# Optimization experiments

Measured on AMD Instinct MI355X. Metric: run time of the kernel, lower is better.

Reference implementation:

```python
import jax
import jax.numpy as jnp
import numpy as np

# Module configuration (matches init_kwargs)
N, C, H, W = 8, 256, 64, 64
CO, KH, KW = 256, 3, 3
SH, SW = 1, 1
PH, PW = 1, 1
DH, DW = 1, 1
G, DG = 1, 1
K = KH * KW
HO = (H + 2 * PH - (DH * (KH - 1) + 1)) // SH + 1
WO = (W + 2 * PW - (DW * (KW - 1) + 1)) // SW + 1


def setup_inputs() -> dict:
    key = jax.random.key(0)
    k1, k2, k3, k4 = jax.random.split(key, 4)
    x = jax.random.normal(k1, (N, C, H, W), dtype=jnp.float32)
    offset = jax.random.normal(k2, (N, DG * 2 * K, HO, WO), dtype=jnp.float32)
    mask = jax.random.uniform(k3, (N, DG * K, HO, WO), dtype=jnp.float32)
    stdv = 1.0 / np.sqrt(C * KH * KW)
    weight = jax.random.uniform(k4, (CO, C // G, KH, KW), dtype=jnp.float32,
                                minval=-stdv, maxval=stdv)
    return {"x": x, "offset": offset, "mask": mask, "weight": weight}


def _deform_sample(x, offset, mask):
    """Modulated deformable bilinear sampling (DCNv2 im2col).

    Returns columns [N, C, K, HO, WO].
    """
    Cg = C // DG
    # offset layout: [N, DG, K, 2(y,x), HO, WO]
    off = offset.reshape(N, DG, K, 2, HO, WO)
    off_y, off_x = off[:, :, :, 0], off[:, :, :, 1]

    # Base sampling grid per kernel tap: [K, HO, WO] broadcastable
    kgy = (jnp.repeat(jnp.arange(KH), KW) * DH).astype(jnp.float32)  # [K]
    kgx = (jnp.tile(jnp.arange(KW), KH) * DW).astype(jnp.float32)    # [K]
    oy = (jnp.arange(HO) * SH - PH).astype(jnp.float32)              # [HO]
    ox = (jnp.arange(WO) * SW - PW).astype(jnp.float32)              # [WO]
    py = kgy[:, None, None] + oy[None, :, None] + off_y  # [N,DG,K,HO,WO]
    px = kgx[:, None, None] + ox[None, None, :] + off_x  # [N,DG,K,HO,WO]

    y0 = jnp.floor(py)
    x0 = jnp.floor(px)
    ly = py - y0
    lx = px - x0
    y0i = y0.astype(jnp.int32)
    x0i = x0.astype(jnp.int32)
    y1i = y0i + 1
    x1i = x0i + 1

    xf = x.reshape(N, DG, Cg, H * W)

    def gather_one(xf_nd, idx_nd):
        # xf_nd: [Cg, H*W], idx_nd: [K*HO*WO] -> [Cg, K*HO*WO]
        return xf_nd[:, idx_nd]

    gather = jax.vmap(jax.vmap(gather_one))  # over N, DG

    def corner(yi, xi, wgt):
        valid = (yi >= 0) & (yi < H) & (xi >= 0) & (xi < W)
        yc = jnp.clip(yi, 0, H - 1)
        xc = jnp.clip(xi, 0, W - 1)
        idx = (yc * W + xc).reshape(N, DG, K * HO * WO)
        g = gather(xf, idx).reshape(N, DG, Cg, K, HO, WO)
        w = (wgt * valid.astype(x.dtype))[:, :, None]  # [N,DG,1,K,HO,WO]
        return g * w

    cols = corner(y0i, x0i, (1.0 - ly) * (1.0 - lx))
    cols = cols + corner(y0i, x1i, (1.0 - ly) * lx)
    cols = cols + corner(y1i, x0i, ly * (1.0 - lx))
    cols = cols + corner(y1i, x1i, ly * lx)

    # modulation
    m = mask.reshape(N, DG, 1, K, HO, WO)
    cols = cols * m
    return cols.reshape(N, C, K, HO, WO)


def reference(x, offset, mask, weight):
    cols = _deform_sample(x, offset, mask)              # [N,C,K,HO,WO]
    colsg = cols.reshape(N, G, C // G, K, HO, WO)
    wg = weight.reshape(G, CO // G, C // G, K)
    out = jnp.einsum('ngckhw,gock->ngohw', colsg, wg)
    return out.reshape(N, CO, HO, WO)
```

## Files before the change

### kernel.cpp

```cpp
#include <hip/hip_runtime.h>
#include <hip/hip_bf16.h>
#include <hip/hip_fp16.h>
#include <stdint.h>

#define N_   8
#define C_   256
#define H_   64
#define W_   64
#define CO_  256
#define K_   9
#define HO_  64
#define WO_  64
#define CK_  (C_ * K_)
#define P_   (HO_ * WO_)

#define BN   128
#define BK   64
#define NT   36
#define NTHR 512

typedef __attribute__((ext_vector_type(8))) _Float16 f16x8;
typedef __attribute__((ext_vector_type(4))) float f32x4;

__device__ __forceinline__ unsigned short f2bf(float f) {
    uint32_t u = __builtin_bit_cast(uint32_t, f);
    uint32_t r = (u + 0x7FFFu + ((u >> 16) & 1u)) >> 16;
    return (unsigned short)r;
}
__device__ __forceinline__ float bf2f(unsigned short u) {
    return __builtin_bit_cast(float, (uint32_t)u << 16);
}
__device__ __forceinline__ unsigned short f2h(float f) {
    return __builtin_bit_cast(unsigned short, (_Float16)f);
}


__global__ __launch_bounds__(256)
void transpose_x(const float* __restrict__ x, unsigned short* __restrict__ xT) {
    __shared__ float t[64][65];
    const int n  = blockIdx.z;
    const int c0 = blockIdx.y * 64;
    const int h0 = blockIdx.x * 64;
    const int tx = threadIdx.x & 63;
    const int ty = threadIdx.x >> 6;
    const float* xp = x + ((size_t)n * C_ + c0) * P_ + h0;
    #pragma unroll
    for (int i = 0; i < 16; ++i) {
        int c = ty * 16 + i;
        t[c][tx] = xp[(size_t)c * P_ + tx];
    }
    __syncthreads();
    unsigned short* op = xT + ((size_t)n * P_ + h0) * C_ + c0;
    #pragma unroll
    for (int i = 0; i < 16; ++i) {
        int hw = ty * 16 + i;
        op[(size_t)hw * C_ + tx] = f2h(t[tx][hw]);
    }
}

__global__ __launch_bounds__(256)
void reorder_w(const float* __restrict__ w, unsigned short* __restrict__ Wt) {
    const int co = blockIdx.x;
    const int c  = threadIdx.x;
    const float* src = w + (size_t)co * CK_ + (size_t)c * K_;
    float v[9];
    #pragma unroll
    for (int k = 0; k < 9; ++k) v[k] = src[k];
    #pragma unroll
    for (int k = 0; k < 9; ++k)
        Wt[(size_t)co * CK_ + k * C_ + c] = f2h(v[k]);
}

__device__ __forceinline__ void barrier_lgkm_only() {
    __builtin_amdgcn_sched_barrier(0);
    asm volatile("s_waitcnt lgkmcnt(0)" ::: "memory");
    __builtin_amdgcn_s_barrier();
    __builtin_amdgcn_sched_barrier(0);
}

#define COMB(dst, A, B, Cc, D) do {                                   \
    __half2 _v = __hmul2(W0, __builtin_bit_cast(__half2, (A)));       \
    _v = __hfma2(W1, __builtin_bit_cast(__half2, (B)), _v);           \
    _v = __hfma2(W2, __builtin_bit_cast(__half2, (Cc)), _v);          \
    _v = __hfma2(W3, __builtin_bit_cast(__half2, (D)), _v);           \
    (dst) = __builtin_bit_cast(unsigned, _v); } while (0)

__global__ __launch_bounds__(NTHR, 2)
void dcn_main(const unsigned short* __restrict__ xT,
              const unsigned short* __restrict__ Wt,
              const float* __restrict__ offset,
              const float* __restrict__ mask,
              float* __restrict__ out) {
    __shared__ uint2 sIdx[BN * K_];
    __shared__ uint4 sWd [BN * K_];
    __shared__ unsigned short sWs[2][CO_ * BK];
    __shared__ unsigned short sBs[2][BN * BK];

    const int tid = threadIdx.x;
    const int bid = blockIdx.x;
    const int n   = bid & 7;
    const int p0  = (bid >> 3) * BN;

    for (int e = tid; e < BN * K_; e += NTHR) {
        int pl = e / K_;
        int k  = e - pl * K_;
        int p  = p0 + pl;
        int ho = p >> 6, wo = p & 63;
        float offy = offset[(size_t)((n * 2 * K_ + 2 * k)     * P_) + p];
        float offx = offset[(size_t)((n * 2 * K_ + 2 * k + 1) * P_) + p];
        float m    = mask  [(size_t)((n * K_ + k) * P_) + p];
        float py = (float)(k / 3 + ho - 1) + offy;
        float px = (float)(k % 3 + wo - 1) + offx;
        float y0f = floorf(py), x0f = floorf(px);
        float ly = py - y0f,   lx = px - x0f;
        int y0 = (int)y0f, x0 = (int)x0f;
        int y1 = y0 + 1,   x1 = x0 + 1;
        bool vy0 = (y0 >= 0) & (y0 < H_);
        bool vy1 = (y1 >= 0) & (y1 < H_);
        bool vx0 = (x0 >= 0) & (x0 < W_);
        bool vx1 = (x1 >= 0) & (x1 < W_);
        float w00 = (1.f - ly) * (1.f - lx) * m * ((vy0 & vx0) ? 1.f : 0.f);
        float w01 = (1.f - ly) * lx         * m * ((vy0 & vx1) ? 1.f : 0.f);
        float w10 = ly * (1.f - lx)         * m * ((vy1 & vx0) ? 1.f : 0.f);
        float w11 = ly * lx                 * m * ((vy1 & vx1) ? 1.f : 0.f);
        unsigned int cy0 = (unsigned)min(max(y0, 0), H_ - 1);
        unsigned int cy1 = (unsigned)min(max(y1, 0), H_ - 1);
        unsigned int cx0 = (unsigned)min(max(x0, 0), W_ - 1);
        unsigned int cx1 = (unsigned)min(max(x1, 0), W_ - 1);
        sIdx[e] = make_uint2((cy0 * W_ + cx0) | ((cy0 * W_ + cx1) << 16),
                             (cy1 * W_ + cx0) | ((cy1 * W_ + cx1) << 16));
        sWd[e] = make_uint4((unsigned)f2h(w00) * 0x10001u,
                            (unsigned)f2h(w01) * 0x10001u,
                            (unsigned)f2h(w10) * 0x10001u,
                            (unsigned)f2h(w11) * 0x10001u);
    }
    __syncthreads();

    const unsigned short* xTn = xT + (size_t)n * P_ * C_;

    const int spl  = tid >> 2;
    const int cs16 = (tid & 3) * 16;
    const int bsw  = spl & 7;
    const int boff0 = spl * 128 + ((((tid & 3) * 2)     ^ bsw) << 4);
    const int boff1 = spl * 128 + ((((tid & 3) * 2 + 1) ^ bsw) << 4);
    const int wco  = tid >> 1;
    const int wchq = (tid & 1) * 4;
    const int wswz = wco & 7;
    const int woff = wco * 128;
    const unsigned short* wsrcbase = Wt + (size_t)wco * CK_ + (tid & 1) * 32;

    const int lane = tid & 63;
    const int wid  = tid >> 6;
    const int wm   = (wid & 3) * 64;
    const int wp   = (wid >> 2) * 64;
    const int l15  = lane & 15;
    const int l4   = lane >> 4;
    const int slA  = l4 ^ (l15 & 7);

    f32x4 acc[4][4] = {};

    uint4 qa0, qa1, qb0, qb1, qc0, qc1, qd0, qd1;
    uint4 wq0, wq1, wq2, wq3;

#define PREF(TT) {                                                        \
        const int kn  = (TT) >> 2;                                        \
        const int c0n = ((TT) & 3) * 64;                                  \
        const unsigned short* ws = wsrcbase + kn * C_ + c0n;              \
        wq0 = *(const uint4*)(ws);                                        \
        wq1 = *(const uint4*)(ws + 8);                                    \
        wq2 = *(const uint4*)(ws + 16);                                   \
        wq3 = *(const uint4*)(ws + 24);                                   \
        uint2 id = sIdx[spl * K_ + kn];                                   \
        const unsigned short* base = xTn + c0n + cs16;                    \
        const unsigned short* ba = base + ((size_t)(id.x & 0xFFFFu) << 8);\
        const unsigned short* bb = base + ((size_t)(id.x >> 16)     << 8);\
        const unsigned short* bc = base + ((size_t)(id.y & 0xFFFFu) << 8);\
        const unsigned short* bd = base + ((size_t)(id.y >> 16)     << 8);\
        qa0 = *(const uint4*)(ba); qa1 = *(const uint4*)(ba + 8);         \
        qb0 = *(const uint4*)(bb); qb1 = *(const uint4*)(bb + 8);         \
        qc0 = *(const uint4*)(bc); qc1 = *(const uint4*)(bc + 8);         \
        qd0 = *(const uint4*)(bd); qd1 = *(const uint4*)(bd + 8);         \
    }

#define STAGE(TT, WB, BB) {                                               \
        asm volatile("s_waitcnt vmcnt(0)" ::: "memory");                  \
        char* wrB = (char*)(WB) + woff;                                   \
        *(uint4*)(wrB + (((wchq + 0) ^ wswz) << 4)) = wq0;                \
        *(uint4*)(wrB + (((wchq + 1) ^ wswz) << 4)) = wq1;                \
        *(uint4*)(wrB + (((wchq + 2) ^ wswz) << 4)) = wq2;                \
        *(uint4*)(wrB + (((wchq + 3) ^ wswz) << 4)) = wq3;                \
        uint4 wv = sWd[spl * K_ + ((TT) >> 2)];                           \
        __half2 W0 = __builtin_bit_cast(__half2, wv.x);                   \
        __half2 W1 = __builtin_bit_cast(__half2, wv.y);                   \
        __half2 W2 = __builtin_bit_cast(__half2, wv.z);                   \
        __half2 W3 = __builtin_bit_cast(__half2, wv.w);                   \
        uint4 r0, r1;                                                     \
        COMB(r0.x, qa0.x, qb0.x, qc0.x, qd0.x);                           \
        COMB(r0.y, qa0.y, qb0.y, qc0.y, qd0.y);                           \
        COMB(r0.z, qa0.z, qb0.z, qc0.z, qd0.z);                           \
        COMB(r0.w, qa0.w, qb0.w, qc0.w, qd0.w);                           \
        COMB(r1.x, qa1.x, qb1.x, qc1.x, qd1.x);                           \
        COMB(r1.y, qa1.y, qb1.y, qc1.y, qd1.y);                           \
        COMB(r1.z, qa1.z, qb1.z, qc1.z, qd1.z);                           \
        COMB(r1.w, qa1.w, qb1.w, qc1.w, qd1.w);                           \
        *(uint4*)((char*)(BB) + boff0) = r0;                              \
        *(uint4*)((char*)(BB) + boff1) = r1;                              \
    }

    PREF(0)
    STAGE(0, sWs[0], sBs[0])
    PREF(1)

    for (int t = 0; t < NT; ++t) {
        const int br = t & 1;
        const int bw = br ^ 1;
        const char* wR = (const char*)sWs[br];
        const char* bR = (const char*)sBs[br];

        barrier_lgkm_only();

        f16x8 a0[2], a1[2], a2[2], a3[2], b0[2], b1[2], b2[2], b3[2];
        {
            const int sl = slA;
            b0[0] = *(const f16x8*)(bR + (wp      + l15) * 128 + (sl << 4));
            b1[0] = *(const f16x8*)(bR + (wp + 16 + l15) * 128 + (sl << 4));
            b2[0] = *(const f16x8*)(bR + (wp + 32 + l15) * 128 + (sl << 4));
            b3[0] = *(const f16x8*)(bR + (wp + 48 + l15) * 128 + (sl << 4));
            a0[0] = *(const f16x8*)(wR + (wm      + l15) * 128 + (sl << 4));
            a1[0] = *(const f16x8*)(wR + (wm + 16 + l15) * 128 + (sl << 4));
            a2[0] = *(const f16x8*)(wR + (wm + 32 + l15) * 128 + (sl << 4));
            a3[0] = *(const f16x8*)(wR + (wm + 48 + l15) * 128 + (sl << 4));
        }

        if (t + 1 < NT) {
            if (br) { STAGE(t + 1, sWs[0], sBs[0]) }
            else    { STAGE(t + 1, sWs[1], sBs[1]) }
            if (t + 2 < NT) PREF(t + 2)
        }

        {
            const int sl = slA ^ 4;
            b0[1] = *(const f16x8*)(bR + (wp      + l15) * 128 + (sl << 4));
            b1[1] = *(const f16x8*)(bR + (wp + 16 + l15) * 128 + (sl << 4));
            b2[1] = *(const f16x8*)(bR + (wp + 32 + l15) * 128 + (sl << 4));
            b3[1] = *(const f16x8*)(bR + (wp + 48 + l15) * 128 + (sl << 4));
            a0[1] = *(const f16x8*)(wR + (wm      + l15) * 128 + (sl << 4));
            a1[1] = *(const f16x8*)(wR + (wm + 16 + l15) * 128 + (sl << 4));
            a2[1] = *(const f16x8*)(wR + (wm + 32 + l15) * 128 + (sl << 4));
            a3[1] = *(const f16x8*)(wR + (wm + 48 + l15) * 128 + (sl << 4));
        }

        #pragma unroll
        for (int ks = 0; ks < 2; ++ks) {
            acc[0][0] = __builtin_amdgcn_mfma_f32_16x16x32_f16(a0[ks], b0[ks], acc[0][0], 0, 0, 0);
            acc[0][1] = __builtin_amdgcn_mfma_f32_16x16x32_f16(a0[ks], b1[ks], acc[0][1], 0, 0, 0);
            acc[0][2] = __builtin_amdgcn_mfma_f32_16x16x32_f16(a0[ks], b2[ks], acc[0][2], 0, 0, 0);
            acc[0][3] = __builtin_amdgcn_mfma_f32_16x16x32_f16(a0[ks], b3[ks], acc[0][3], 0, 0, 0);
            acc[1][0] = __builtin_amdgcn_mfma_f32_16x16x32_f16(a1[ks], b0[ks], acc[1][0], 0, 0, 0);
            acc[1][1] = __builtin_amdgcn_mfma_f32_16x16x32_f16(a1[ks], b1[ks], acc[1][1], 0, 0, 0);
            acc[1][2] = __builtin_amdgcn_mfma_f32_16x16x32_f16(a1[ks], b2[ks], acc[1][2], 0, 0, 0);
            acc[1][3] = __builtin_amdgcn_mfma_f32_16x16x32_f16(a1[ks], b3[ks], acc[1][3], 0, 0, 0);
            acc[2][0] = __builtin_amdgcn_mfma_f32_16x16x32_f16(a2[ks], b0[ks], acc[2][0], 0, 0, 0);
            acc[2][1] = __builtin_amdgcn_mfma_f32_16x16x32_f16(a2[ks], b1[ks], acc[2][1], 0, 0, 0);
            acc[2][2] = __builtin_amdgcn_mfma_f32_16x16x32_f16(a2[ks], b2[ks], acc[2][2], 0, 0, 0);
            acc[2][3] = __builtin_amdgcn_mfma_f32_16x16x32_f16(a2[ks], b3[ks], acc[2][3], 0, 0, 0);
            acc[3][0] = __builtin_amdgcn_mfma_f32_16x16x32_f16(a3[ks], b0[ks], acc[3][0], 0, 0, 0);
            acc[3][1] = __builtin_amdgcn_mfma_f32_16x16x32_f16(a3[ks], b1[ks], acc[3][1], 0, 0, 0);
            acc[3][2] = __builtin_amdgcn_mfma_f32_16x16x32_f16(a3[ks], b2[ks], acc[3][2], 0, 0, 0);
            acc[3][3] = __builtin_amdgcn_mfma_f32_16x16x32_f16(a3[ks], b3[ks], acc[3][3], 0, 0, 0);
        }
    }
#undef PREF
#undef STAGE

    float* outn = out + (size_t)n * CO_ * P_;
    #pragma unroll
    for (int m = 0; m < 4; ++m) {
        int co = wm + m * 16 + l4 * 4;
        #pragma unroll
        for (int nn = 0; nn < 4; ++nn) {
            int p = p0 + wp + nn * 16 + l15;
            #pragma unroll
            for (int r = 0; r < 4; ++r) {
                outn[(size_t)(co + r) * P_ + p] = acc[m][nn][r];
            }
        }
    }
}

template <int TAG>
__global__ __launch_bounds__(512, 2)
void dcn_fb(const float* __restrict__ x,
            const float* __restrict__ offset,
            const float* __restrict__ mask,
            const float* __restrict__ weight,
            float* __restrict__ out) {
    typedef __attribute__((ext_vector_type(8))) short bf16x8;
    __shared__ uint2  sIdx[128 * K_];
    __shared__ float4 sW  [128 * K_];
    __shared__ unsigned short sWs[CO_ * 32];
    __shared__ unsigned short sBs[128 * 32];

    const int tid = threadIdx.x;
    const int n  = blockIdx.y;
    const int p0 = blockIdx.x * 128;

    for (int e = tid; e < 128 * K_; e += 512) {
        int pl = e / K_;
        int k  = e - pl * K_;
        int p  = p0 + pl;
        int ho = p >> 6, wo = p & 63;
        float offy = offset[(size_t)((n * 2 * K_ + 2 * k)     * P_) + p];
        float offx = offset[(size_t)((n * 2 * K_ + 2 * k + 1) * P_) + p];
        float m    = mask  [(size_t)((n * K_ + k) * P_) + p];
        float py = (float)(k / 3 + ho - 1) + offy;
        float px = (float)(k % 3 + wo - 1) + offx;
        float y0f = floorf(py), x0f = floorf(px);
        float ly = py - y0f,   lx = px - x0f;
        int y0 = (int)y0f, x0 = (int)x0f;
        int y1 = y0 + 1,   x1 = x0 + 1;
        bool vy0 = (y0 >= 0) & (y0 < H_);
        bool vy1 = (y1 >= 0) & (y1 < H_);
        bool vx0 = (x0 >= 0) & (x0 < W_);
        bool vx1 = (x1 >= 0) & (x1 < W_);
        float w00 = (1.f - ly) * (1.f - lx) * m * ((vy0 & vx0) ? 1.f : 0.f);
        float w01 = (1.f - ly) * lx         * m * ((vy0 & vx1) ? 1.f : 0.f);
        float w10 = ly * (1.f - lx)         * m * ((vy1 & vx0) ? 1.f : 0.f);
        float w11 = ly * lx                 * m * ((vy1 & vx1) ? 1.f : 0.f);
        unsigned int cy0 = (unsigned)min(max(y0, 0), H_ - 1);
        unsigned int cy1 = (unsigned)min(max(y1, 0), H_ - 1);
        unsigned int cx0 = (unsigned)min(max(x0, 0), W_ - 1);
        unsigned int cx1 = (unsigned)min(max(x1, 0), W_ - 1);
        sIdx[e] = make_uint2((cy0 * W_ + cx0) | ((cy0 * W_ + cx1) << 16),
                             (cy1 * W_ + cx0) | ((cy1 * W_ + cx1) << 16));
        sW[e]   = make_float4(w00, w01, w10, w11);
    }

    const float* xn = x + (size_t)n * C_ * P_;
    const int pl   = tid >> 2;
    const int pl9  = pl * K_;
    const int ckb  = (tid & 3) * 8;
    const int wco  = tid >> 1;
    const int wck  = (tid & 1) * 16;

    const int lane = tid & 63;
    const int wid  = tid >> 6;
    const int wm   = (wid & 1) * 128;
    const int wp   = (wid >> 1) * 32;
    const int l15  = lane & 15;
    const int l4   = lane >> 4;

    f32x4 acc[8][2] = {};

    for (int ck0 = 0; ck0 < CK_; ck0 += 32) {
        __syncthreads();
        {
            const float4* wsrc = (const float4*)(weight + (size_t)wco * CK_ + ck0 + wck);
            float4 wa = wsrc[0], wb = wsrc[1], wc = wsrc[2], wd = wsrc[3];
            uint4 q0, q1;
            q0.x = f2bf(wa.x) | ((unsigned)f2bf(wa.y) << 16);
            q0.y = f2bf(wa.z) | ((unsigned)f2bf(wa.w) << 16);
            q0.z = f2bf(wb.x) | ((unsigned)f2bf(wb.y) << 16);
            q0.w = f2bf(wb.z) | ((unsigned)f2bf(wb.w) << 16);
            q1.x = f2bf(wc.x) | ((unsigned)f2bf(wc.y) << 16);
            q1.y = f2bf(wc.z) | ((unsigned)f2bf(wc.w) << 16);
            q1.z = f2bf(wd.x) | ((unsigned)f2bf(wd.y) << 16);
            q1.w = f2bf(wd.z) | ((unsigned)f2bf(wd.w) << 16);
            *(uint4*)&sWs[wco * 32 + wck]     = q0;
            *(uint4*)&sWs[wco * 32 + wck + 8] = q1;
        }
        {
            int ckstart = ck0 + ckb;
            int cc = ckstart / 9;
            int kk = ckstart - cc * 9;
            unsigned int packed[4];
            unsigned short colv[8];
            #pragma unroll
            for (int j = 0; j < 8; ++j) {
                int e = pl9 + kk;
                uint2  id = sIdx[e];
                float4 wv = sW[e];
                const float* xp = xn + ((size_t)cc << 12);
                float v = wv.x * xp[id.x & 0xFFFFu]
                        + wv.y * xp[id.x >> 16]
                        + wv.z * xp[id.y & 0xFFFFu]
                        + wv.w * xp[id.y >> 16];
                colv[j] = f2bf(v);
                ++kk; if (kk == 9) { kk = 0; ++cc; }
            }
            packed[0] = colv[0] | ((unsigned)colv[1] << 16);
            packed[1] = colv[2] | ((unsigned)colv[3] << 16);
            packed[2] = colv[4] | ((unsigned)colv[5] << 16);
            packed[3] = colv[6] | ((unsigned)colv[7] << 16);
            *(uint4*)&sBs[pl * 32 + ckb] = *(uint4*)packed;
        }
        __syncthreads();
        bf16x8 bfr0 = *(const bf16x8*)&sBs[(wp + l15)      * 32 + l4 * 8];
        bf16x8 bfr1 = *(const bf16x8*)&sBs[(wp + 16 + l15) * 32 + l4 * 8];
        #pragma unroll
        for (int m = 0; m < 8; ++m) {
            bf16x8 afr = *(const bf16x8*)&sWs[(wm + m * 16 + l15) * 32 + l4 * 8];
            acc[m][0] = __builtin_amdgcn_mfma_f32_16x16x32_bf16(afr, bfr0, acc[m][0], 0, 0, 0);
            acc[m][1] = __builtin_amdgcn_mfma_f32_16x16x32_bf16(afr, bfr1, acc[m][1], 0, 0, 0);
        }
    }

    float* outn = out + (size_t)n * CO_ * P_;
    #pragma unroll
    for (int m = 0; m < 8; ++m) {
        int co = wm + m * 16 + l4 * 4;
        #pragma unroll
        for (int nn = 0; nn < 2; ++nn) {
            int p = p0 + wp + nn * 16 + l15;
            #pragma unroll
            for (int r = 0; r < 4; ++r) {
                outn[(size_t)(co + r) * P_ + p] = acc[m][nn][r];
            }
        }
    }
}

extern "C" void kernel_launch(void* const* d_in, const int* in_sizes, int n_in,
                              void* d_out, int out_size, void* d_ws, size_t ws_size,
                              hipStream_t stream) {
    const float* x      = (const float*)d_in[0];
    const float* offset = (const float*)d_in[1];
    const float* mask   = (const float*)d_in[2];
    const float* weight = (const float*)d_in[3];
    float* out = (float*)d_out;

    const size_t xT_elems = (size_t)N_ * P_ * C_;
    const size_t Wt_elems = (size_t)CO_ * CK_;
    const size_t need     = (xT_elems + Wt_elems) * sizeof(unsigned short);

    if (ws_size >= need) {
        unsigned short* xT = (unsigned short*)d_ws;
        unsigned short* Wt = xT + xT_elems;
        transpose_x<<<dim3(P_ / 64, C_ / 64, N_), dim3(256), 0, stream>>>(x, xT);
        reorder_w<<<dim3(CO_), dim3(256), 0, stream>>>(weight, Wt);
        dcn_main<<<dim3((P_ / BN) * N_), dim3(NTHR), 0, stream>>>(xT, Wt, offset, mask, out);
    } else if (ws_size >= (8u << 20)) {
        dcn_fb<1><<<dim3(P_ / 128, N_), dim3(512), 0, stream>>>(x, offset, mask, weight, out);
    } else {
        dcn_fb<0><<<dim3(P_ / 128, N_), dim3(512), 0, stream>>>(x, offset, mask, weight, out);
    }
}
```

Baseline: 72.29 us.

## Double block threads to 1024 with smaller per-warp tiles and gather work

Raises the main kernel's block size from 512 to 1024 threads, splitting the 256-channel by 128-pixel tile across 16 waves of 32x64 instead of 8 waves of 64x64. Each thread now gathers and combines one 16-byte chunk per corner instead of two and loads two weight vectors instead of four, which cuts per-thread register use so more waves can be resident. The explicit vmcnt wait before staging is removed and the MFMAs for the first k-half are issued before the second-half LDS reads. The cost is more waves contending at each barrier, less register-level reuse of fragments per wave, and a launch bound of 1024 threads with 4 blocks per CU that the LDS footprint may not allow.

Measured after the change: 68.97 us. -4.6%, faster.

```diff
diff --git a/kernel.cpp b/kernel.cpp
--- a/kernel.cpp
+++ b/kernel.cpp
@@ -17,7 +17,7 @@
 #define BN   128
 #define BK   64
 #define NT   36
-#define NTHR 512
+#define NTHR 1024
 
 typedef __attribute__((ext_vector_type(8))) _Float16 f16x8;
 typedef __attribute__((ext_vector_type(4))) float f32x4;
@@ -85,7 +85,7 @@
     _v = __hfma2(W3, __builtin_bit_cast(__half2, (D)), _v);           \
     (dst) = __builtin_bit_cast(unsigned, _v); } while (0)
 
-__global__ __launch_bounds__(NTHR, 2)
+__global__ __launch_bounds__(NTHR, 4)
 void dcn_main(const unsigned short* __restrict__ xT,
               const unsigned short* __restrict__ Wt,
               const float* __restrict__ offset,
@@ -138,73 +138,57 @@
 
     const unsigned short* xTn = xT + (size_t)n * P_ * C_;
 
-    const int spl  = tid >> 2;
-    const int cs16 = (tid & 3) * 16;
-    const int bsw  = spl & 7;
-    const int boff0 = spl * 128 + ((((tid & 3) * 2)     ^ bsw) << 4);
-    const int boff1 = spl * 128 + ((((tid & 3) * 2 + 1) ^ bsw) << 4);
-    const int wco  = tid >> 1;
-    const int wchq = (tid & 1) * 4;
+    const int spl = tid >> 3;
+    const int cs  = tid & 7;
+    const int boff = spl * 128 + ((cs ^ (spl & 7)) << 4);
+    const int wco  = tid >> 2;
+    const int wsl  = tid & 3;
     const int wswz = wco & 7;
     const int woff = wco * 128;
-    const unsigned short* wsrcbase = Wt + (size_t)wco * CK_ + (tid & 1) * 32;
+    const unsigned short* wsrcbase = Wt + (size_t)wco * CK_ + wsl * 8;
 
     const int lane = tid & 63;
     const int wid  = tid >> 6;
-    const int wm   = (wid & 3) * 64;
-    const int wp   = (wid >> 2) * 64;
+    const int wm   = (wid & 7) * 32;
+    const int wp   = (wid >> 3) * 64;
     const int l15  = lane & 15;
     const int l4   = lane >> 4;
     const int slA  = l4 ^ (l15 & 7);
 
-    f32x4 acc[4][4] = {};
-
-    uint4 qa0, qa1, qb0, qb1, qc0, qc1, qd0, qd1;
-    uint4 wq0, wq1, wq2, wq3;
+    f32x4 acc[2][4] = {};
+
+    uint4 qa, qb, qc, qd;
+    uint4 wq0, wq1;
 
 #define PREF(TT) {                                                        \
         const int kn  = (TT) >> 2;                                        \
         const int c0n = ((TT) & 3) * 64;                                  \
         const unsigned short* ws = wsrcbase + kn * C_ + c0n;              \
         wq0 = *(const uint4*)(ws);                                        \
-        wq1 = *(const uint4*)(ws + 8);                                    \
-        wq2 = *(const uint4*)(ws + 16);                                   \
-        wq3 = *(const uint4*)(ws + 24);                                   \
+        wq1 = *(const uint4*)(ws + 32);                                   \
         uint2 id = sIdx[spl * K_ + kn];                                   \
-        const unsigned short* base = xTn + c0n + cs16;                    \
-        const unsigned short* ba = base + ((size_t)(id.x & 0xFFFFu) << 8);\
-        const unsigned short* bb = base + ((size_t)(id.x >> 16)     << 8);\
-        const unsigned short* bc = base + ((size_t)(id.y & 0xFFFFu) << 8);\
-        const unsigned short* bd = base + ((size_t)(id.y >> 16)     << 8);\
-        qa0 = *(const uint4*)(ba); qa1 = *(const uint4*)(ba + 8);         \
-        qb0 = *(const uint4*)(bb); qb1 = *(const uint4*)(bb + 8);         \
-        qc0 = *(const uint4*)(bc); qc1 = *(const uint4*)(bc + 8);         \
-        qd0 = *(const uint4*)(bd); qd1 = *(const uint4*)(bd + 8);         \
+        const unsigned short* base = xTn + c0n + cs * 8;                  \
+        qa = *(const uint4*)(base + ((size_t)(id.x & 0xFFFFu) << 8));     \
+        qb = *(const uint4*)(base + ((size_t)(id.x >> 16)     << 8));     \
+        qc = *(const uint4*)(base + ((size_t)(id.y & 0xFFFFu) << 8));     \
+        qd = *(const uint4*)(base + ((size_t)(id.y >> 16)     << 8));     \
     }
 
 #define STAGE(TT, WB, BB) {                                               \
-        asm volatile("s_waitcnt vmcnt(0)" ::: "memory");                  \
         char* wrB = (char*)(WB) + woff;                                   \
-        *(uint4*)(wrB + (((wchq + 0) ^ wswz) << 4)) = wq0;                \
-        *(uint4*)(wrB + (((wchq + 1) ^ wswz) << 4)) = wq1;                \
-        *(uint4*)(wrB + (((wchq + 2) ^ wswz) << 4)) = wq2;                \
-        *(uint4*)(wrB + (((wchq + 3) ^ wswz) << 4)) = wq3;                \
+        *(uint4*)(wrB + ((wsl       ^ wswz) << 4)) = wq0;                 \
+        *(uint4*)(wrB + (((wsl + 4) ^ wswz) << 4)) = wq1;                 \
         uint4 wv = sWd[spl * K_ + ((TT) >> 2)];                           \
         __half2 W0 = __builtin_bit_cast(__half2, wv.x);                   \
         __half2 W1 = __builtin_bit_cast(__half2, wv.y);                   \
         __half2 W2 = __builtin_bit_cast(__half2, wv.z);                   \
         __half2 W3 = __builtin_bit_cast(__half2, wv.w);                   \
-        uint4 r0, r1;                                                     \
-        COMB(r0.x, qa0.x, qb0.x, qc0.x, qd0.x);                           \
-        COMB(r0.y, qa0.y, qb0.y, qc0.y, qd0.y);                           \
-        COMB(r0.z, qa0.z, qb0.z, qc0.z, qd0.z);                           \
-        COMB(r0.w, qa0.w, qb0.w, qc0.w, qd0.w);                           \
-        COMB(r1.x, qa1.x, qb1.x, qc1.x, qd1.x);                           \
-        COMB(r1.y, qa1.y, qb1.y, qc1.y, qd1.y);                           \
-        COMB(r1.z, qa1.z, qb1.z, qc1.z, qd1.z);                           \
-        COMB(r1.w, qa1.w, qb1.w, qc1.w, qd1.w);                           \
-        *(uint4*)((char*)(BB) + boff0) = r0;                              \
-        *(uint4*)((char*)(BB) + boff1) = r1;                              \
+        uint4 r;                                                          \
+        COMB(r.x, qa.x, qb.x, qc.x, qd.x);                                \
+        COMB(r.y, qa.y, qb.y, qc.y, qd.y);                                \
+        COMB(r.z, qa.z, qb.z, qc.z, qd.z);                                \
+        COMB(r.w, qa.w, qb.w, qc.w, qd.w);                                \
+        *(uint4*)((char*)(BB) + boff) = r;                                \
     }
 
     PREF(0)
@@ -213,23 +197,20 @@
 
     for (int t = 0; t < NT; ++t) {
         const int br = t & 1;
-        const int bw = br ^ 1;
         const char* wR = (const char*)sWs[br];
         const char* bR = (const char*)sBs[br];
 
         barrier_lgkm_only();
 
-        f16x8 a0[2], a1[2], a2[2], a3[2], b0[2], b1[2], b2[2], b3[2];
+        f16x8 A0, A1, B0, B1, B2, B3;
         {
             const int sl = slA;
-            b0[0] = *(const f16x8*)(bR + (wp      + l15) * 128 + (sl << 4));
-            b1[0] = *(const f16x8*)(bR + (wp + 16 + l15) * 128 + (sl << 4));
-            b2[0] = *(const f16x8*)(bR + (wp + 32 + l15) * 128 + (sl << 4));
-            b3[0] = *(const f16x8*)(bR + (wp + 48 + l15) * 128 + (sl << 4));
-            a0[0] = *(const f16x8*)(wR + (wm      + l15) * 128 + (sl << 4));
-            a1[0] = *(const f16x8*)(wR + (wm + 16 + l15) * 128 + (sl << 4));
-            a2[0] = *(const f16x8*)(wR + (wm + 32 + l15) * 128 + (sl << 4));
-            a3[0] = *(const f16x8*)(wR + (wm + 48 + l15) * 128 + (sl << 4));
+            B0 = *(const f16x8*)(bR + (wp      + l15) * 128 + (sl << 4));
+            B1 = *(const f16x8*)(bR + (wp + 16 + l15) * 128 + (sl << 4));
+            B2 = *(const f16x8*)(bR + (wp + 32 + l15) * 128 + (sl << 4));
+            B3 = *(const f16x8*)(bR + (wp + 48 + l15) * 128 + (sl << 4));
+            A0 = *(const f16x8*)(wR + (wm      + l15) * 128 + (sl << 4));
+            A1 = *(const f16x8*)(wR + (wm + 16 + l15) * 128 + (sl << 4));
         }
 
         if (t + 1 < NT) {
@@ -238,44 +219,39 @@
             if (t + 2 < NT) PREF(t + 2)
         }
 
+        acc[0][0] = __builtin_amdgcn_mfma_f32_16x16x32_f16(A0, B0, acc[0][0], 0, 0, 0);
+        acc[0][1] = __builtin_amdgcn_mfma_f32_16x16x32_f16(A0, B1, acc[0][1], 0, 0, 0);
+        acc[0][2] = __builtin_amdgcn_mfma_f32_16x16x32_f16(A0, B2, acc[0][2], 0, 0, 0);
+        acc[0][3] = __builtin_amdgcn_mfma_f32_16x16x32_f16(A0, B3, acc[0][3], 0, 0, 0);
+        acc[1][0] = __builtin_amdgcn_mfma_f32_16x16x32_f16(A1, B0, acc[1][0], 0, 0, 0);
+        acc[1][1] = __builtin_amdgcn_mfma_f32_16x16x32_f16(A1, B1, acc[1][1], 0, 0, 0);
+        acc[1][2] = __builtin_amdgcn_mfma_f32_16x16x32_f16(A1, B2, acc[1][2], 0, 0, 0);
+        acc[1][3] = __builtin_amdgcn_mfma_f32_16x16x32_f16(A1, B3, acc[1][3], 0, 0, 0);
+
         {
             const int sl = slA ^ 4;
-            b0[1] = *(const f16x8*)(bR + (wp      + l15) * 128 + (sl << 4));
-            b1[1] = *(const f16x8*)(bR + (wp + 16 + l15) * 128 + (sl << 4));
-            b2[1] = *(const f16x8*)(bR + (wp + 32 + l15) * 128 + (sl << 4));
-            b3[1] = *(const f16x8*)(bR + (wp + 48 + l15) * 128 + (sl << 4));
-            a0[1] = *(const f16x8*)(wR + (wm      + l15) * 128 + (sl << 4));
-            a1[1] = *(const f16x8*)(wR + (wm + 16 + l15) * 128 + (sl << 4));
-            a2[1] = *(const f16x8*)(wR + (wm + 32 + l15) * 128 + (sl << 4));
-            a3[1] = *(const f16x8*)(wR + (wm + 48 + l15) * 128 + (sl << 4));
-        }
-
-        #pragma unroll
-        for (int ks = 0; ks < 2; ++ks) {
-            acc[0][0] = __builtin_amdgcn_mfma_f32_16x16x32_f16(a0[ks], b0[ks], acc[0][0], 0, 0, 0);
-            acc[0][1] = __builtin_amdgcn_mfma_f32_16x16x32_f16(a0[ks], b1[ks], acc[0][1], 0, 0, 0);
-            acc[0][2] = __builtin_amdgcn_mfma_f32_16x16x32_f16(a0[ks], b2[ks], acc[0][2], 0, 0, 0);
-            acc[0][3] = __builtin_amdgcn_mfma_f32_16x16x32_f16(a0[ks], b3[ks], acc[0][3], 0, 0, 0);
-            acc[1][0] = __builtin_amdgcn_mfma_f32_16x16x32_f16(a1[ks], b0[ks], acc[1][0], 0, 0, 0);
-            acc[1][1] = __builtin_amdgcn_mfma_f32_16x16x32_f16(a1[ks], b1[ks], acc[1][1], 0, 0, 0);
-            acc[1][2] = __builtin_amdgcn_mfma_f32_16x16x32_f16(a1[ks], b2[ks], acc[1][2], 0, 0, 0);
-            acc[1][3] = __builtin_amdgcn_mfma_f32_16x16x32_f16(a1[ks], b3[ks], acc[1][3], 0, 0, 0);
-            acc[2][0] = __builtin_amdgcn_mfma_f32_16x16x32_f16(a2[ks], b0[ks], acc[2][0], 0, 0, 0);
-            acc[2][1] = __builtin_amdgcn_mfma_f32_16x16x32_f16(a2[ks], b1[ks], acc[2][1], 0, 0, 0);
-            acc[2][2] = __builtin_amdgcn_mfma_f32_16x16x32_f16(a2[ks], b2[ks], acc[2][2], 0, 0, 0);
-            acc[2][3] = __builtin_amdgcn_mfma_f32_16x16x32_f16(a2[ks], b3[ks], acc[2][3], 0, 0, 0);
-            acc[3][0] = __builtin_amdgcn_mfma_f32_16x16x32_f16(a3[ks], b0[ks], acc[3][0], 0, 0, 0);
-            acc[3][1] = __builtin_amdgcn_mfma_f32_16x16x32_f16(a3[ks], b1[ks], acc[3][1], 0, 0, 0);
-            acc[3][2] = __builtin_amdgcn_mfma_f32_16x16x32_f16(a3[ks], b2[ks], acc[3][2], 0, 0, 0);
-            acc[3][3] = __builtin_amdgcn_mfma_f32_16x16x32_f16(a3[ks], b3[ks], acc[3][3], 0, 0, 0);
-        }
+            B0 = *(const f16x8*)(bR + (wp      + l15) * 128 + (sl << 4));
+            B1 = *(const f16x8*)(bR + (wp + 16 + l15) * 128 + (sl << 4));
+            B2 = *(const f16x8*)(bR + (wp + 32 + l15) * 128 + (sl << 4));
+            B3 = *(const f16x8*)(bR + (wp + 48 + l15) * 128 + (sl << 4));
+            A0 = *(const f16x8*)(wR + (wm      + l15) * 128 + (sl << 4));
+            A1 = *(const f16x8*)(wR + (wm + 16 + l15) * 128 + (sl << 4));
+        }
+        acc[0][0] = __builtin_amdgcn_mfma_f32_16x16x32_f16(A0, B0, acc[0][0], 0, 0, 0);
+        acc[0][1] = __builtin_amdgcn_mfma_f32_16x16x32_f16(A0, B1, acc[0][1], 0, 0, 0);
+        acc[0][2] = __builtin_amdgcn_mfma_f32_16x16x32_f16(A0, B2, acc[0][2], 0, 0, 0);
+        acc[0][3] = __builtin_amdgcn_mfma_f32_16x16x32_f16(A0, B3, acc[0][3], 0, 0, 0);
+        acc[1][0] = __builtin_amdgcn_mfma_f32_16x16x32_f16(A1, B0, acc[1][0], 0, 0, 0);
+        acc[1][1] = __builtin_amdgcn_mfma_f32_16x16x32_f16(A1, B1, acc[1][1], 0, 0, 0);
+        acc[1][2] = __builtin_amdgcn_mfma_f32_16x16x32_f16(A1, B2, acc[1][2], 0, 0, 0);
+        acc[1][3] = __builtin_amdgcn_mfma_f32_16x16x32_f16(A1, B3, acc[1][3], 0, 0, 0);
     }
 #undef PREF
 #undef STAGE
 
     float* outn = out + (size_t)n * CO_ * P_;
     #pragma unroll
-    for (int m = 0; m < 4; ++m) {
+    for (int m = 0; m < 2; ++m) {
         int co = wm + m * 16 + l4 * 4;
         #pragma unroll
         for (int nn = 0; nn < 4; ++nn) {
```
